# Kernel tuning notes

Hardware: AMD Instinct MI355X
Metric: run time of the kernel (lower is better)

## Reference

```python
import jax, jax.numpy as jnp
import numpy as np

N = 50000   # nodes
E = 800000  # edges
G = 64      # graphs in batch
EPS = 1e-5  # BatchNorm eps


def setup_inputs() -> dict:
    key = jax.random.key(0)
    ks = jax.random.split(key, 32)
    inp = {
        'x': jax.random.normal(ks[0], (N, 1), jnp.float32),
        'edge_index': jax.random.randint(ks[1], (2, E), 0, N),
        'batch': jnp.sort(jax.random.randint(ks[2], (N,), 0, G)),
    }
    dims = [(1, 64), (64, 64), (64, 64), (64, 64)]
    for i, (din, dout) in enumerate(dims, 1):
        inp[f'W{i}'] = jax.random.normal(ks[2 + i], (din, dout), jnp.float32) / np.sqrt(din)
        inp[f'b{i}'] = jnp.zeros((dout,), jnp.float32)
        inp[f'g{i}'] = jnp.ones((dout,), jnp.float32)
        inp[f'bt{i}'] = jnp.zeros((dout,), jnp.float32)
    inp['fw1'] = jax.random.normal(ks[10], (128, 64), jnp.float32) / 8.0
    inp['fb1'] = jnp.zeros((128,), jnp.float32)
    inp['fw2'] = jax.random.normal(ks[11], (10, 128), jnp.float32) / np.sqrt(128)
    inp['fb2'] = jnp.zeros((10,), jnp.float32)
    return inp


def _gcn_norm(edge_index):
    # add self-loops, symmetric normalization (PyG GCNConv default)
    loop = jnp.arange(N)
    row = jnp.concatenate([edge_index[0], loop])
    col = jnp.concatenate([edge_index[1], loop])
    deg = jax.ops.segment_sum(jnp.ones_like(col, jnp.float32), col, num_segments=N)
    dinv = jnp.where(deg > 0, deg ** -0.5, 0.0)
    norm = dinv[row] * dinv[col]
    return row, col, norm


def _gcn(x, W, b, row, col, norm):
    h = x @ W                                   # [N, dout]
    msg = h[row] * norm[:, None]                # gather + scale per edge
    agg = jax.ops.segment_sum(msg, col, num_segments=N)  # scatter-add
    return agg + b


def _bn(x, g, bt):
    m = x.mean(0)
    v = x.var(0)
    return g * (x - m) * jax.lax.rsqrt(v + EPS) + bt


def reference(x, edge_index, batch,
              W1, b1, g1, bt1, W2, b2, g2, bt2,
              W3, b3, g3, bt3, W4, b4, g4, bt4,
              fw1, fb1, fw2, fb2):
    row, col, norm = _gcn_norm(edge_index)
    x = jax.nn.relu(_bn(_gcn(x, W1, b1, row, col, norm), g1, bt1))
    x = jax.nn.relu(_bn(_gcn(x, W2, b2, row, col, norm), g2, bt2))
    x = jax.nn.relu(_bn(_gcn(x, W3, b3, row, col, norm), g3, bt3))
    x = jax.nn.relu(_bn(_gcn(x, W4, b4, row, col, norm), g4, bt4))
    # global mean pool over graphs
    cnt = jax.ops.segment_sum(jnp.ones((N,), jnp.float32), batch, num_segments=G)
    pooled = jax.ops.segment_sum(x, batch, num_segments=G) / jnp.clip(cnt, 1.0)[:, None]
    h = jax.nn.relu(pooled @ fw1.T + fb1)
    return h @ fw2.T + fb2
```

## Files before the change

kernel.cpp:

```cpp
#include <hip/hip_runtime.h>
#include <hip/hip_fp16.h>

#define NN 50000
#define NE 800000
#define NG 64
#define FD 64
#define BN_EPS 1e-5f
#define SCAN_B 256
#define NBIN 98
#define BINCAP 12288
#define SCH 4096
#define SCH_NBLK ((NE + SCH - 1) / SCH)
#define INV_NN (1.0f / NN)
#define MM_NBLK ((NN + 3) / 4)

__global__ __launch_bounds__(256) void k_binscatter(const int* __restrict__ row,
                                                    const int* __restrict__ col,
                                                    int* __restrict__ gcnt,
                                                    int* __restrict__ bins) {
    __shared__ int stage[SCH];
    __shared__ unsigned char stageb[SCH];
    __shared__ int cnt[NBIN], off[NBIN], cur[NBIN], gbase[NBIN];
    int t = threadIdx.x;
    int e0 = blockIdx.x * SCH;
    int nk = NE - e0; if (nk > SCH) nk = SCH;
    if (nk <= 0) return;
    for (int b = t; b < NBIN; b += 256) cnt[b] = 0;
    __syncthreads();
    for (int k = t; k < nk; k += 256) {
        int c = col[e0 + k];
        atomicAdd(&cnt[c >> 9], 1);
    }
    __syncthreads();
    if (t == 0) {
        int run = 0;
        for (int b = 0; b < NBIN; ++b) { off[b] = run; run += cnt[b]; }
    }
    __syncthreads();
    if (t < NBIN) {
        cur[t] = off[t];
        gbase[t] = t * BINCAP + atomicAdd(&gcnt[t], cnt[t]);
    }
    __syncthreads();
    for (int k = t; k < nk; k += 256) {
        int c = col[e0 + k];
        int r = row[e0 + k];
        int b = c >> 9;
        int pos = atomicAdd(&cur[b], 1);
        stage[pos] = ((c & 511) << 16) | r;
        stageb[pos] = (unsigned char)b;
    }
    __syncthreads();
    for (int k = t; k < nk; k += 256) {
        int b = stageb[k];
        bins[gbase[b] + (k - off[b])] = stage[k];
    }
}

__global__ __launch_bounds__(256) void k_binscan(const int* __restrict__ gcnt,
                                                 const int* __restrict__ bins,
                                                 const float* __restrict__ x,
                                                 int* __restrict__ cursor,
                                                 int* __restrict__ bsum,
                                                 float* __restrict__ dinv,
                                                 float* __restrict__ xd) {
    __shared__ int ldeg[512];
    __shared__ int psc[256];
    int b = blockIdx.x, t = threadIdx.x;
    for (int l = t; l < 512; l += 256) ldeg[l] = 0;
    __syncthreads();
    int nb = gcnt[b];
    const int* bp = bins + b * BINCAP;
    for (int k = t; k < nb; k += 256) atomicAdd(&ldeg[bp[k] >> 16], 1);
    __syncthreads();
    int d0 = ldeg[2 * t], d1 = ldeg[2 * t + 1];
    int pv = d0 + d1;
    psc[t] = pv;
    __syncthreads();
    for (int off = 1; off < 256; off <<= 1) {
        int u = (t >= off) ? psc[t - off] : 0;
        __syncthreads();
        psc[t] += u;
        __syncthreads();
    }
    int excl = psc[t] - pv;
    int base = b << 9;
    int i0 = base + 2 * t, i1 = i0 + 1;
    if (i0 < NN) {
        cursor[i0] = excl;
        float dv = rsqrtf((float)d0 + 1.0f);
        dinv[i0] = dv; xd[i0] = x[i0] * dv;
    }
    if (i1 < NN) {
        cursor[i1] = excl + d0;
        float dv = rsqrtf((float)d1 + 1.0f);
        dinv[i1] = dv; xd[i1] = x[i1] * dv;
    }
    if (t == 255) bsum[b] = psc[255];
}

__global__ __launch_bounds__(SCAN_B) void k_scan_top(int* __restrict__ bsum,
                                                     float* __restrict__ stats) {
    __shared__ int sh[SCAN_B];
    int t = threadIdx.x;
    if (t < 2) stats[t] = 0.0f;
    int v = (t < NBIN) ? bsum[t] : 0;
    sh[t] = v;
    __syncthreads();
    for (int off = 1; off < SCAN_B; off <<= 1) {
        int u = (t >= off) ? sh[t - off] : 0;
        __syncthreads();
        sh[t] += u;
        __syncthreads();
    }
    if (t < NBIN) bsum[t] = sh[t] - v;
}

__global__ __launch_bounds__(256) void k_binfill_l1(const int* __restrict__ gcnt,
                                                    const int* __restrict__ bins,
                                                    const int* __restrict__ cursor,
                                                    const int* __restrict__ bsum,
                                                    int* __restrict__ eidx,
                                                    const float* __restrict__ xd,
                                                    const float* __restrict__ x,
                                                    const float* __restrict__ dinv,
                                                    float* __restrict__ s,
                                                    float* __restrict__ stats) {
    __shared__ int lstart[512], lcur[512];
    __shared__ float ls[256], lq[256];
    int b = blockIdx.x, t = threadIdx.x;
    int base = b << 9;
    int bofs = bsum[b];
    for (int l = t; l < 512; l += 256) {
        int i = base + l;
        int st = (i < NN) ? cursor[i] + bofs : 0;
        lstart[l] = st; lcur[l] = st;
    }
    __syncthreads();
    int nb = gcnt[b];
    const int* bp = bins + b * BINCAP;
    for (int k = t; k < nb; k += 256) {
        int v = bp[k];
        int pos = atomicAdd(&lcur[v >> 16], 1);
        eidx[pos] = v & 0xFFFF;
    }
    __syncthreads();
    float a = 0.0f, q = 0.0f;
    #pragma unroll
    for (int half = 0; half < 2; ++half) {
        int l = t + half * 256;
        int i = base + l;
        if (i < NN) {
            float acc = 0.0f;
            int e0 = lstart[l], e1 = lcur[l];
            for (int k = e0; k < e1; ++k) acc += xd[eidx[k]];
            float di = dinv[i];
            float sv = di * (acc + di * x[i]);
            s[i] = sv;
            a += sv; q += sv * sv;
        }
    }
    ls[t] = a; lq[t] = q;
    __syncthreads();
    for (int st = 128; st > 0; st >>= 1) {
        if (t < st) { ls[t] += ls[t + st]; lq[t] += lq[t + st]; }
        __syncthreads();
    }
    if (t == 0) { atomicAdd(&stats[0], ls[0]); atomicAdd(&stats[1], lq[0]); }
}

__global__ __launch_bounds__(256) void k_mm_l1(const float* __restrict__ s,
                                               const float* __restrict__ stats,
                                               const float* __restrict__ W1,
                                               const float* __restrict__ g1,
                                               const float* __restrict__ bt1,
                                               const float* __restrict__ W,
                                               __half* __restrict__ h) {
    __shared__ float Ws[64 * 64];
    __shared__ float xs[4 * 64];
    __shared__ float als[64], cls[64];
    int t = threadIdx.x;
    for (int k = t; k < 64 * 64; k += 256) Ws[k] = W[k];
    if (t < 64) {
        float mean = stats[0] * INV_NN;
        float var  = stats[1] * INV_NN - mean * mean;
        float w = W1[t];
        float rinv = rsqrtf(var * w * w + BN_EPS);
        float a = g1[t] * w * rinv;
        als[t] = a;
        cls[t] = bt1[t] - a * mean;
    }
    __syncthreads();
    int n0 = blockIdx.x * 4;
    int j = t & 63, n = t >> 6;
    int node = n0 + n;
    float sv = (node < NN) ? s[node] : 0.0f;
    xs[t] = fmaxf(als[j] * sv + cls[j], 0.0f);
    __syncthreads();
    if (node < NN) {
        float acc = 0.f;
        #pragma unroll
        for (int k = 0; k < 64; ++k) acc += xs[n * 64 + k] * Ws[k * 64 + j];
        h[node * 64 + j] = __float2half(acc);
    }
}

__global__ __launch_bounds__(256) void k_mm_bn(const float* __restrict__ src,
                                               const float* __restrict__ bnsum,
                                               const float* __restrict__ bnsq,
                                               const float* __restrict__ g,
                                               const float* __restrict__ bt,
                                               const float* __restrict__ W,
                                               __half* __restrict__ h) {
    __shared__ float Ws[64 * 64];
    __shared__ float xs[4 * 64];
    __shared__ float scl[64], shf[64];
    int t = threadIdx.x;
    for (int k = t; k < 64 * 64; k += 256) Ws[k] = W[k];
    if (t < 64) {
        float mean = bnsum[t] * INV_NN;
        float var  = bnsq[t] * INV_NN - mean * mean;
        float rinv = rsqrtf(var + BN_EPS);
        float sc = g[t] * rinv;
        scl[t] = sc;
        shf[t] = bt[t] - sc * mean;
    }
    __syncthreads();
    int n0 = blockIdx.x * 4;
    int j = t & 63, n = t >> 6;
    int node = n0 + n;
    int gidx = n0 * 64 + t;
    float v = (gidx < NN * 64) ? src[gidx] : 0.0f;
    xs[t] = fmaxf(scl[j] * v + shf[j], 0.0f);
    __syncthreads();
    if (node < NN) {
        float acc = 0.f;
        #pragma unroll
        for (int k = 0; k < 64; ++k) acc += xs[n * 64 + k] * Ws[k * 64 + j];
        h[node * 64 + j] = __float2half(acc);
    }
}

__global__ __launch_bounds__(256) void k_gather(const int* __restrict__ cursor,
                                                const int* __restrict__ bsum,
                                                const int* __restrict__ eidx,
                                                const float* __restrict__ dinv,
                                                const __half* __restrict__ h,
                                                const float* __restrict__ b,
                                                float* __restrict__ agg,
                                                float* __restrict__ bnsumz,
                                                float* __restrict__ bnsqz) {
    if (blockIdx.x == 0) {
        int t = threadIdx.x;
        if (t < 64) bnsumz[t] = 0.0f;
        else if (t < 128) bnsqz[t - 64] = 0.0f;
    }
    int node = blockIdx.x * 4 + (threadIdx.x >> 6);
    if (node >= NN) return;
    int lane = threadIdx.x & 63;
    int eslot = lane >> 4;
    int fb = (lane & 15) << 2;
    int start = cursor[node] + bsum[node >> 9];
    int end = (node < NN - 1) ? cursor[node + 1] + bsum[(node + 1) >> 9] : NE;
    float4 acc0 = make_float4(0.f, 0.f, 0.f, 0.f);
    float4 acc1 = make_float4(0.f, 0.f, 0.f, 0.f);
    int e = start + eslot;
    for (; e + 4 < end; e += 8) {
        int r0 = eidx[e], r1 = eidx[e + 4];
        float dr0 = dinv[r0], dr1 = dinv[r1];
        uint2 u0 = *reinterpret_cast<const uint2*>(&h[r0 * 64 + fb]);
        uint2 u1 = *reinterpret_cast<const uint2*>(&h[r1 * 64 + fb]);
        float2 a01 = __half22float2(*reinterpret_cast<__half2*>(&u0.x));
        float2 a23 = __half22float2(*reinterpret_cast<__half2*>(&u0.y));
        float2 b01 = __half22float2(*reinterpret_cast<__half2*>(&u1.x));
        float2 b23 = __half22float2(*reinterpret_cast<__half2*>(&u1.y));
        acc0.x += a01.x * dr0; acc0.y += a01.y * dr0; acc0.z += a23.x * dr0; acc0.w += a23.y * dr0;
        acc1.x += b01.x * dr1; acc1.y += b01.y * dr1; acc1.z += b23.x * dr1; acc1.w += b23.y * dr1;
    }
    if (e < end) {
        int r = eidx[e];
        float dr = dinv[r];
        uint2 u0 = *reinterpret_cast<const uint2*>(&h[r * 64 + fb]);
        float2 a01 = __half22float2(*reinterpret_cast<__half2*>(&u0.x));
        float2 a23 = __half22float2(*reinterpret_cast<__half2*>(&u0.y));
        acc0.x += a01.x * dr; acc0.y += a01.y * dr; acc0.z += a23.x * dr; acc0.w += a23.y * dr;
    }
    acc0.x += acc1.x; acc0.y += acc1.y; acc0.z += acc1.z; acc0.w += acc1.w;
    acc0.x += __shfl_xor(acc0.x, 16); acc0.y += __shfl_xor(acc0.y, 16);
    acc0.z += __shfl_xor(acc0.z, 16); acc0.w += __shfl_xor(acc0.w, 16);
    acc0.x += __shfl_xor(acc0.x, 32); acc0.y += __shfl_xor(acc0.y, 32);
    acc0.z += __shfl_xor(acc0.z, 32); acc0.w += __shfl_xor(acc0.w, 32);
    if (lane < 16) {
        float dc = dinv[node];
        uint2 u0 = *reinterpret_cast<const uint2*>(&h[node * 64 + fb]);
        float2 s01 = __half22float2(*reinterpret_cast<__half2*>(&u0.x));
        float2 s23 = __half22float2(*reinterpret_cast<__half2*>(&u0.y));
        const float4 bv = *reinterpret_cast<const float4*>(&b[fb]);
        float4 o;
        o.x = dc * (acc0.x + dc * s01.x) + bv.x;
        o.y = dc * (acc0.y + dc * s01.y) + bv.y;
        o.z = dc * (acc0.z + dc * s23.x) + bv.z;
        o.w = dc * (acc0.w + dc * s23.y) + bv.w;
        *reinterpret_cast<float4*>(&agg[node * 64 + fb]) = o;
    }
}

__global__ __launch_bounds__(256) void k_bn_stats(const float* __restrict__ agg,
                                                  float* __restrict__ bnsum, float* __restrict__ bnsq,
                                                  float* __restrict__ pooledz, float* __restrict__ cntz) {
    if (pooledz != nullptr && blockIdx.x == 0) {
        for (int k = threadIdx.x; k < 64 * 64; k += 256) pooledz[k] = 0.0f;
        if (threadIdx.x < 64) cntz[threadIdx.x] = 0.0f;
    }
    __shared__ float ls[256], lq[256];
    int j = threadIdx.x & 63, nl = threadIdx.x >> 6;
    float a = 0.f, b = 0.f;
    for (int i = blockIdx.x * 4 + nl; i < NN; i += gridDim.x * 4) {
        float v = agg[i * 64 + j]; a += v; b += v * v;
    }
    ls[threadIdx.x] = a; lq[threadIdx.x] = b; __syncthreads();
    if (threadIdx.x < 128) { ls[threadIdx.x] += ls[threadIdx.x + 128]; lq[threadIdx.x] += lq[threadIdx.x + 128]; }
    __syncthreads();
    if (threadIdx.x < 64) {
        atomicAdd(&bnsum[j], ls[threadIdx.x] + ls[threadIdx.x + 64]);
        atomicAdd(&bnsq[j],  lq[threadIdx.x] + lq[threadIdx.x + 64]);
    }
}

__global__ __launch_bounds__(256) void k_pool_bn(const float* __restrict__ agg,
                                                 const float* __restrict__ bnsum,
                                                 const float* __restrict__ bnsq,
                                                 const float* __restrict__ g4,
                                                 const float* __restrict__ bt4,
                                                 const int* __restrict__ batch,
                                                 float* __restrict__ pooled,
                                                 float* __restrict__ cnt) {
    const int wpb = 4;
    int wave = blockIdx.x * wpb + (threadIdx.x >> 6);
    int lane = threadIdx.x & 63;
    const int nwaves = gridDim.x * wpb;
    int chunk = (NN + nwaves - 1) / nwaves;
    int i0 = wave * chunk;
    int i1 = i0 + chunk; if (i1 > NN) i1 = NN;
    if (i0 >= NN) return;
    float mean = bnsum[lane] * INV_NN;
    float var  = bnsq[lane] * INV_NN - mean * mean;
    float rinv = rsqrtf(var + BN_EPS);
    float sc = g4[lane] * rinv;
    float sh = bt4[lane] - sc * mean;
    float acc = 0.0f;
    int curb = batch[i0];
    int runlen = 0;
    for (int i = i0; i < i1; ++i) {
        int b = batch[i];
        if (b != curb) {
            atomicAdd(&pooled[curb * 64 + lane], acc);
            if (lane == 0) atomicAdd(&cnt[curb], (float)runlen);
            acc = 0.0f; runlen = 0; curb = b;
        }
        acc += fmaxf(sc * agg[i * 64 + lane] + sh, 0.0f);
        ++runlen;
    }
    atomicAdd(&pooled[curb * 64 + lane], acc);
    if (lane == 0) atomicAdd(&cnt[curb], (float)runlen);
}

__global__ __launch_bounds__(128) void k_fc(const float* __restrict__ pooled, const float* __restrict__ cnt,
                                            const float* __restrict__ fw1, const float* __restrict__ fb1,
                                            const float* __restrict__ fw2, const float* __restrict__ fb2,
                                            float* __restrict__ out) {
    __shared__ float p[64], hsh[128];
    int g = blockIdx.x, t = threadIdx.x;
    if (t < 64) {
        float c = cnt[g]; c = c < 1.f ? 1.f : c;
        p[t] = pooled[g * 64 + t] / c;
    }
    __syncthreads();
    float acc = fb1[t];
    #pragma unroll 8
    for (int k = 0; k < 64; ++k) acc += p[k] * fw1[t * 64 + k];
    hsh[t] = fmaxf(acc, 0.f);
    __syncthreads();
    if (t < 10) {
        float o = fb2[t];
        #pragma unroll 8
        for (int k = 0; k < 128; ++k) o += hsh[k] * fw2[t * 128 + k];
        out[g * 10 + t] = o;
    }
}

extern "C" void kernel_launch(void* const* d_in, const int* in_sizes, int n_in,
                              void* d_out, int out_size, void* d_ws, size_t ws_size,
                              hipStream_t stream) {
    const float* x   = (const float*)d_in[0];
    const int* ei    = (const int*)d_in[1];
    const int* batch = (const int*)d_in[2];
    const float* W[5]  = {nullptr, (const float*)d_in[3],  (const float*)d_in[7],
                                   (const float*)d_in[11], (const float*)d_in[15]};
    const float* bb[5] = {nullptr, (const float*)d_in[4],  (const float*)d_in[8],
                                   (const float*)d_in[12], (const float*)d_in[16]};
    const float* gg[5] = {nullptr, (const float*)d_in[5],  (const float*)d_in[9],
                                   (const float*)d_in[13], (const float*)d_in[17]};
    const float* bt[5] = {nullptr, (const float*)d_in[6],  (const float*)d_in[10],
                                   (const float*)d_in[14], (const float*)d_in[18]};
    const float* fw1 = (const float*)d_in[19];
    const float* fb1 = (const float*)d_in[20];
    const float* fw2 = (const float*)d_in[21];
    const float* fb2 = (const float*)d_in[22];
    float* out = (float*)d_out;

    const int* row = ei;
    const int* col = ei + NE;

    float* ws = (float*)d_ws;
    int*   cursor  = (int*)ws;
    int*   eidx    = (int*)(ws + 50000);
    float* dinv    = ws + 850000;
    float* xd      = ws + 900000;
    int*   bsum    = (int*)(ws + 950000);
    float* s       = ws + 951000;
    float* stats   = ws + 1001008;
    float* bnsum   = ws + 1001072;
    float* bnsq    = ws + 1001136;
    float* pooled  = ws + 1001360;
    float* cnt     = ws + 1005456;
    int*   gcnt    = (int*)(ws + 1056000);
    __half* hbuf   = (__half*)(ws + 1100000);
    int*   bins    = (int*)(ws + 1100000);
    float* aggbuf  = ws + 4300000;

    const int B = 256;

    hipMemsetAsync(gcnt, 0, NBIN * sizeof(int), stream);
    k_binscatter<<<SCH_NBLK, B, 0, stream>>>(row, col, gcnt, bins);
    k_binscan<<<NBIN, B, 0, stream>>>(gcnt, bins, x, cursor, bsum, dinv, xd);
    k_scan_top<<<1, SCAN_B, 0, stream>>>(bsum, stats);
    k_binfill_l1<<<NBIN, B, 0, stream>>>(gcnt, bins, cursor, bsum, eidx, xd, x, dinv, s, stats);

    k_mm_l1<<<MM_NBLK, B, 0, stream>>>(s, stats, W[1], gg[1], bt[1], W[2], hbuf);
    k_gather<<<MM_NBLK, B, 0, stream>>>(cursor, bsum, eidx, dinv, hbuf, bb[2], aggbuf, bnsum, bnsq);
    k_bn_stats<<<512, B, 0, stream>>>(aggbuf, bnsum, bnsq, nullptr, nullptr);

    for (int L = 3; L <= 4; ++L) {
        k_mm_bn<<<MM_NBLK, B, 0, stream>>>(aggbuf, bnsum, bnsq, gg[L - 1], bt[L - 1], W[L], hbuf);
        k_gather<<<MM_NBLK, B, 0, stream>>>(cursor, bsum, eidx, dinv, hbuf, bb[L], aggbuf, bnsum, bnsq);
        k_bn_stats<<<512, B, 0, stream>>>(aggbuf, bnsum, bnsq,
                                          (L == 4) ? pooled : nullptr, (L == 4) ? cnt : nullptr);
    }

    k_pool_bn<<<512, B, 0, stream>>>(aggbuf, bnsum, bnsq, gg[4], bt[4], batch, pooled, cnt);
    k_fc<<<NG, 128, 0, stream>>>(pooled, cnt, fw1, fb1, fw2, fb2, out);
}
```

Measured before the change: 322.9 us.

## Prescale features by source dinv in matmul; widen gather loads to 16B

```diff
diff --git a/kernel.cpp b/kernel.cpp
--- a/kernel.cpp
+++ b/kernel.cpp
@@ -175,6 +175,7 @@
                                                const float* __restrict__ g1,
                                                const float* __restrict__ bt1,
                                                const float* __restrict__ W,
+                                               const float* __restrict__ dinv,
                                                __half* __restrict__ h) {
     __shared__ float Ws[64 * 64];
     __shared__ float xs[4 * 64];
@@ -201,7 +202,7 @@
         float acc = 0.f;
         #pragma unroll
         for (int k = 0; k < 64; ++k) acc += xs[n * 64 + k] * Ws[k * 64 + j];
-        h[node * 64 + j] = __float2half(acc);
+        h[node * 64 + j] = __float2half(acc * dinv[node]);
     }
 }
 
@@ -211,6 +212,7 @@
                                                const float* __restrict__ g,
                                                const float* __restrict__ bt,
                                                const float* __restrict__ W,
+                                               const float* __restrict__ dinv,
                                                __half* __restrict__ h) {
     __shared__ float Ws[64 * 64];
     __shared__ float xs[4 * 64];
@@ -237,7 +239,7 @@
         float acc = 0.f;
         #pragma unroll
         for (int k = 0; k < 64; ++k) acc += xs[n * 64 + k] * Ws[k * 64 + j];
-        h[node * 64 + j] = __float2half(acc);
+        h[node * 64 + j] = __float2half(acc * dinv[node]);
     }
 }
 
@@ -251,57 +253,68 @@
                                                 float* __restrict__ bnsumz,
                                                 float* __restrict__ bnsqz) {
     if (blockIdx.x == 0) {
-        int t = threadIdx.x;
-        if (t < 64) bnsumz[t] = 0.0f;
-        else if (t < 128) bnsqz[t - 64] = 0.0f;
+        int tt = threadIdx.x;
+        if (tt < 64) bnsumz[tt] = 0.0f;
+        else if (tt < 128) bnsqz[tt - 64] = 0.0f;
     }
     int node = blockIdx.x * 4 + (threadIdx.x >> 6);
     if (node >= NN) return;
     int lane = threadIdx.x & 63;
-    int eslot = lane >> 4;
-    int fb = (lane & 15) << 2;
+    int eslot = lane >> 3;
+    int fb = (lane & 7) << 3;
     int start = cursor[node] + bsum[node >> 9];
     int end = (node < NN - 1) ? cursor[node + 1] + bsum[(node + 1) >> 9] : NE;
-    float4 acc0 = make_float4(0.f, 0.f, 0.f, 0.f);
-    float4 acc1 = make_float4(0.f, 0.f, 0.f, 0.f);
+    float a0 = 0.f, a1 = 0.f, a2 = 0.f, a3 = 0.f, a4 = 0.f, a5 = 0.f, a6 = 0.f, a7 = 0.f;
+    float c0 = 0.f, c1 = 0.f, c2 = 0.f, c3 = 0.f, c4 = 0.f, c5 = 0.f, c6 = 0.f, c7 = 0.f;
     int e = start + eslot;
-    for (; e + 4 < end; e += 8) {
-        int r0 = eidx[e], r1 = eidx[e + 4];
-        float dr0 = dinv[r0], dr1 = dinv[r1];
-        uint2 u0 = *reinterpret_cast<const uint2*>(&h[r0 * 64 + fb]);
-        uint2 u1 = *reinterpret_cast<const uint2*>(&h[r1 * 64 + fb]);
-        float2 a01 = __half22float2(*reinterpret_cast<__half2*>(&u0.x));
-        float2 a23 = __half22float2(*reinterpret_cast<__half2*>(&u0.y));
-        float2 b01 = __half22float2(*reinterpret_cast<__half2*>(&u1.x));
-        float2 b23 = __half22float2(*reinterpret_cast<__half2*>(&u1.y));
-        acc0.x += a01.x * dr0; acc0.y += a01.y * dr0; acc0.z += a23.x * dr0; acc0.w += a23.y * dr0;
-        acc1.x += b01.x * dr1; acc1.y += b01.y * dr1; acc1.z += b23.x * dr1; acc1.w += b23.y * dr1;
+    for (; e + 8 < end; e += 16) {
+        int r0 = eidx[e], r1 = eidx[e + 8];
+        uint4 u = *reinterpret_cast<const uint4*>(&h[(r0 << 6) + fb]);
+        uint4 v = *reinterpret_cast<const uint4*>(&h[(r1 << 6) + fb]);
+        float2 p;
+        p = __half22float2(*reinterpret_cast<__half2*>(&u.x)); a0 += p.x; a1 += p.y;
+        p = __half22float2(*reinterpret_cast<__half2*>(&u.y)); a2 += p.x; a3 += p.y;
+        p = __half22float2(*reinterpret_cast<__half2*>(&u.z)); a4 += p.x; a5 += p.y;
+        p = __half22float2(*reinterpret_cast<__half2*>(&u.w)); a6 += p.x; a7 += p.y;
+        p = __half22float2(*reinterpret_cast<__half2*>(&v.x)); c0 += p.x; c1 += p.y;
+        p = __half22float2(*reinterpret_cast<__half2*>(&v.y)); c2 += p.x; c3 += p.y;
+        p = __half22float2(*reinterpret_cast<__half2*>(&v.z)); c4 += p.x; c5 += p.y;
+        p = __half22float2(*reinterpret_cast<__half2*>(&v.w)); c6 += p.x; c7 += p.y;
     }
     if (e < end) {
         int r = eidx[e];
-        float dr = dinv[r];
-        uint2 u0 = *reinterpret_cast<const uint2*>(&h[r * 64 + fb]);
-        float2 a01 = __half22float2(*reinterpret_cast<__half2*>(&u0.x));
-        float2 a23 = __half22float2(*reinterpret_cast<__half2*>(&u0.y));
-        acc0.x += a01.x * dr; acc0.y += a01.y * dr; acc0.z += a23.x * dr; acc0.w += a23.y * dr;
-    }
-    acc0.x += acc1.x; acc0.y += acc1.y; acc0.z += acc1.z; acc0.w += acc1.w;
-    acc0.x += __shfl_xor(acc0.x, 16); acc0.y += __shfl_xor(acc0.y, 16);
-    acc0.z += __shfl_xor(acc0.z, 16); acc0.w += __shfl_xor(acc0.w, 16);
-    acc0.x += __shfl_xor(acc0.x, 32); acc0.y += __shfl_xor(acc0.y, 32);
-    acc0.z += __shfl_xor(acc0.z, 32); acc0.w += __shfl_xor(acc0.w, 32);
-    if (lane < 16) {
+        uint4 u = *reinterpret_cast<const uint4*>(&h[(r << 6) + fb]);
+        float2 p;
+        p = __half22float2(*reinterpret_cast<__half2*>(&u.x)); a0 += p.x; a1 += p.y;
+        p = __half22float2(*reinterpret_cast<__half2*>(&u.y)); a2 += p.x; a3 += p.y;
+        p = __half22float2(*reinterpret_cast<__half2*>(&u.z)); a4 += p.x; a5 += p.y;
+        p = __half22float2(*reinterpret_cast<__half2*>(&u.w)); a6 += p.x; a7 += p.y;
+    }
+    a0 += c0; a1 += c1; a2 += c2; a3 += c3; a4 += c4; a5 += c5; a6 += c6; a7 += c7;
+    #pragma unroll
+    for (int d = 8; d <= 32; d <<= 1) {
+        a0 += __shfl_xor(a0, d); a1 += __shfl_xor(a1, d);
+        a2 += __shfl_xor(a2, d); a3 += __shfl_xor(a3, d);
+        a4 += __shfl_xor(a4, d); a5 += __shfl_xor(a5, d);
+        a6 += __shfl_xor(a6, d); a7 += __shfl_xor(a7, d);
+    }
+    if (eslot == 0) {
         float dc = dinv[node];
-        uint2 u0 = *reinterpret_cast<const uint2*>(&h[node * 64 + fb]);
-        float2 s01 = __half22float2(*reinterpret_cast<__half2*>(&u0.x));
-        float2 s23 = __half22float2(*reinterpret_cast<__half2*>(&u0.y));
-        const float4 bv = *reinterpret_cast<const float4*>(&b[fb]);
-        float4 o;
-        o.x = dc * (acc0.x + dc * s01.x) + bv.x;
-        o.y = dc * (acc0.y + dc * s01.y) + bv.y;
-        o.z = dc * (acc0.z + dc * s23.x) + bv.z;
-        o.w = dc * (acc0.w + dc * s23.y) + bv.w;
-        *reinterpret_cast<float4*>(&agg[node * 64 + fb]) = o;
+        uint4 u = *reinterpret_cast<const uint4*>(&h[(node << 6) + fb]);
+        float2 p;
+        p = __half22float2(*reinterpret_cast<__half2*>(&u.x)); a0 += p.x; a1 += p.y;
+        p = __half22float2(*reinterpret_cast<__half2*>(&u.y)); a2 += p.x; a3 += p.y;
+        p = __half22float2(*reinterpret_cast<__half2*>(&u.z)); a4 += p.x; a5 += p.y;
+        p = __half22float2(*reinterpret_cast<__half2*>(&u.w)); a6 += p.x; a7 += p.y;
+        const float4 bv0 = *reinterpret_cast<const float4*>(&b[fb]);
+        const float4 bv1 = *reinterpret_cast<const float4*>(&b[fb + 4]);
+        float4 o0, o1;
+        o0.x = dc * a0 + bv0.x; o0.y = dc * a1 + bv0.y;
+        o0.z = dc * a2 + bv0.z; o0.w = dc * a3 + bv0.w;
+        o1.x = dc * a4 + bv1.x; o1.y = dc * a5 + bv1.y;
+        o1.z = dc * a6 + bv1.z; o1.w = dc * a7 + bv1.w;
+        *reinterpret_cast<float4*>(&agg[node * 64 + fb]) = o0;
+        *reinterpret_cast<float4*>(&agg[node * 64 + fb + 4]) = o1;
     }
 }
 
@@ -437,12 +450,12 @@
     k_scan_top<<<1, SCAN_B, 0, stream>>>(bsum, stats);
     k_binfill_l1<<<NBIN, B, 0, stream>>>(gcnt, bins, cursor, bsum, eidx, xd, x, dinv, s, stats);
 
-    k_mm_l1<<<MM_NBLK, B, 0, stream>>>(s, stats, W[1], gg[1], bt[1], W[2], hbuf);
+    k_mm_l1<<<MM_NBLK, B, 0, stream>>>(s, stats, W[1], gg[1], bt[1], W[2], dinv, hbuf);
     k_gather<<<MM_NBLK, B, 0, stream>>>(cursor, bsum, eidx, dinv, hbuf, bb[2], aggbuf, bnsum, bnsq);
     k_bn_stats<<<512, B, 0, stream>>>(aggbuf, bnsum, bnsq, nullptr, nullptr);
 
     for (int L = 3; L <= 4; ++L) {
-        k_mm_bn<<<MM_NBLK, B, 0, stream>>>(aggbuf, bnsum, bnsq, gg[L - 1], bt[L - 1], W[L], hbuf);
+        k_mm_bn<<<MM_NBLK, B, 0, stream>>>(aggbuf, bnsum, bnsq, gg[L - 1], bt[L - 1], W[L], dinv, hbuf);
         k_gather<<<MM_NBLK, B, 0, stream>>>(cursor, bsum, eidx, dinv, hbuf, bb[L], aggbuf, bnsum, bnsq);
         k_bn_stats<<<512, B, 0, stream>>>(aggbuf, bnsum, bnsq,
                                           (L == 4) ? pooled : nullptr, (L == 4) ? cnt : nullptr);
```

After: 306.2 us. -5.2%, faster.
